# Optimization experiments

Hardware: AMD Instinct MI355X
Metric: run time of the kernel (lower is better)

The kernel has to match this reference:

```python
import jax, jax.numpy as jnp
import numpy as np

B = 65536   # batch
S = 3       # pad_size / seq len
DIN = 72    # input feature dim
D = 100     # dim_model
H = 10      # num_head
DH = D // H # dim_head = 10
FF = 512    # ffn hidden
L = 8       # encoder layers
CLS = 40    # cls_dim


def _pos_encoding():
    pe = np.array([[pos / 10000.0 ** (i // 2 * 2.0 / D) for i in range(D)]
                   for pos in range(S)], dtype=np.float32)
    pe[:, 0::2] = np.sin(pe[:, 0::2])
    pe[:, 1::2] = np.cos(pe[:, 1::2])
    return jnp.asarray(pe)  # [S, D]


def setup_inputs() -> dict:
    key = jax.random.key(0)
    ks = jax.random.split(key, 24)
    n = lambda k, shape: 0.05 * jax.random.normal(k, shape, dtype=jnp.float32)
    inp = {
        'x': jax.random.normal(ks[0], (B, S, DIN), dtype=jnp.float32),
        'label': jax.random.randint(ks[1], (B,), 0, CLS),
        'fa_label': jax.random.randint(ks[2], (B,), 0, CLS),
        'We': n(ks[3], (D, DIN)), 'be': n(ks[4], (D,)),
        'pe': _pos_encoding(),
        'Wq': n(ks[5], (L, D, D)), 'bq': n(ks[6], (L, D)),
        'Wk': n(ks[7], (L, D, D)), 'bk': n(ks[8], (L, D)),
        'Wv': n(ks[9], (L, D, D)), 'bv': n(ks[10], (L, D)),
        'Wo': n(ks[11], (L, D, D)), 'bo': n(ks[12], (L, D)),
        'ln1_g': jnp.ones((L, D), jnp.float32), 'ln1_b': jnp.zeros((L, D), jnp.float32),
        'W1': n(ks[13], (L, FF, D)), 'b1': n(ks[14], (L, FF)),
        'W2': n(ks[15], (L, D, FF)), 'b2': n(ks[16], (L, D)),
        'ln2_g': jnp.ones((L, D), jnp.float32), 'ln2_b': jnp.zeros((L, D), jnp.float32),
        'Wf': n(ks[17], (CLS, S * D)), 'bf': n(ks[18], (CLS,)),
    }
    return inp


def _ln(x, g, b, eps=1e-5):
    m = x.mean(-1, keepdims=True)
    v = ((x - m) ** 2).mean(-1, keepdims=True)
    return (x - m) / jnp.sqrt(v + eps) * g + b


def _forward(x, We, be, pe, Wq, bq, Wk, bk, Wv, bv, Wo, bo,
             ln1_g, ln1_b, W1, b1, W2, b2, ln2_g, ln2_b, Wf, bf):
    Bsz = x.shape[0]
    out = x @ We.T + be          # [B, S, D] embedding
    out = out + pe               # positional encoding (dropout = identity in eval)
    scale = DH ** -0.5
    for i in range(L):
        xin = out
        Q = xin @ Wq[i].T + bq[i]
        K = xin @ Wk[i].T + bk[i]
        V = xin @ Wv[i].T + bv[i]
        # Faithful row-major reshape (original uses .view, which interleaves
        # seq and head dims rather than a transpose-based head split).
        Qh = Q.reshape(Bsz * H, -1, DH)   # [B*H, S, DH]
        Kh = K.reshape(Bsz * H, -1, DH)
        Vh = V.reshape(Bsz * H, -1, DH)
        attn = jax.nn.softmax(jnp.einsum('bqd,bkd->bqk', Qh, Kh) * scale, axis=-1)
        ctx = jnp.einsum('bqk,bkd->bqd', attn, Vh).reshape(Bsz, -1, D)
        out = _ln(ctx @ Wo[i].T + bo[i] + xin, ln1_g[i], ln1_b[i])
        # position-wise FFN
        h = jax.nn.relu(out @ W1[i].T + b1[i])
        out = _ln(h @ W2[i].T + b2[i] + out, ln2_g[i], ln2_b[i])
    out = out.reshape(Bsz, S * D) @ Wf.T + bf   # [B, CLS]
    return out


def reference(x, label, fa_label, We, be, pe, Wq, bq, Wk, bk, Wv, bv, Wo, bo,
              ln1_g, ln1_b, W1, b1, W2, b2, ln2_g, ln2_b, Wf, bf):
    # label / fa_label are unused in the original forward
    return _forward(x, We, be, pe, Wq, bq, Wk, bk, Wv, bv, Wo, bo,
                    ln1_g, ln1_b, W1, b1, W2, b2, ln2_g, ln2_b, Wf, bf)
```

## Files before the change

kernel.cpp:

```cpp
#include <hip/hip_runtime.h>
#include <hip/hip_bf16.h>


typedef __attribute__((ext_vector_type(8))) short short8;
typedef __attribute__((ext_vector_type(4))) float floatx4;

namespace {
constexpr int S = 3, DIN = 72, D = 100, FF = 512, L = 8, CLS = 40;
constexpr int NB = 16, R = 48, NT = 256;
constexpr int LDA = 136;
constexpr int LDH = 200;
constexpr float SCALE = 0.3162277660168379f;

constexpr int PL_QKVO = 7 * 4 * 512;
constexpr int WQ_OFF = 0;
constexpr int WK_OFF = WQ_OFF + L * PL_QKVO;
constexpr int WV_OFF = WK_OFF + L * PL_QKVO;
constexpr int WO_OFF = WV_OFF + L * PL_QKVO;
constexpr int PL_W1 = 32 * 4 * 512;
constexpr int W1_OFF = WO_OFF + L * PL_QKVO;
constexpr int PL_W2 = 7 * 16 * 512;
constexpr int W2_OFF = W1_OFF + L * PL_W1;
constexpr int WE_OFF = W2_OFF + L * PL_W2;
}

__device__ __forceinline__ unsigned short f2bf(float f) {
  unsigned int u = __float_as_uint(f);
  u = u + 0x7fffu + ((u >> 16) & 1u);
  return (unsigned short)(u >> 16);
}

__device__ __forceinline__ unsigned pkbf(float a, float b) {
  __hip_bfloat162 h = __float22bfloat162_rn(make_float2(a, b));
  return *reinterpret_cast<unsigned*>(&h);
}

__device__ __forceinline__ void st_bf4(unsigned short* p, floatx4 v) {
  *reinterpret_cast<uint2*>(p) = make_uint2(pkbf(v.x, v.y), pkbf(v.z, v.w));
}

__device__ __forceinline__ void load10(float* o, const unsigned short* p) {
  const unsigned* u = (const unsigned*)p;
#pragma unroll
  for (int w = 0; w < 5; ++w) {
    unsigned x = u[w];
    o[2 * w] = __uint_as_float(x << 16);
    o[2 * w + 1] = __uint_as_float(x & 0xffff0000u);
  }
}

__device__ __forceinline__ void ldwf4(const unsigned short* base, short8* o) {
#pragma unroll
  for (int ks = 0; ks < 4; ++ks) o[ks] = *(const short8*)(base + ks * 512);
}

__device__ __forceinline__ void ln_rows(float* xrow, const float* srow,
                                        const float* __restrict__ g,
                                        const float* __restrict__ b,
                                        unsigned short* sArow, int ln,
                                        int cnt) {
  floatx4 v[7];
  float sum = 0.f;
#pragma unroll
  for (int i = 0; i < 7; ++i)
    if (i < cnt) {
      const int col = i * 16 + ln * 4;
      floatx4 t = *(const floatx4*)(xrow + col) + *(const floatx4*)(srow + col);
      v[i] = t;
      sum += t.x + t.y + t.z + t.w;
    }
  sum += __shfl_xor(sum, 1, 4);
  sum += __shfl_xor(sum, 2, 4);
  const float mean = sum * 0.01f;
  float var = 0.f;
#pragma unroll
  for (int i = 0; i < 7; ++i)
    if (i < cnt) {
      floatx4 d = v[i] - mean;
      var += d.x * d.x + d.y * d.y + d.z * d.z + d.w * d.w;
    }
  var += __shfl_xor(var, 1, 4);
  var += __shfl_xor(var, 2, 4);
  const float rstd = rsqrtf(var * 0.01f + 1e-5f);
#pragma unroll
  for (int i = 0; i < 7; ++i)
    if (i < cnt) {
      const int col = i * 16 + ln * 4;
      floatx4 o = (v[i] - mean) * rstd * *(const floatx4*)(g + col) +
                  *(const floatx4*)(b + col);
      *(floatx4*)(xrow + col) = o;
      st_bf4(sArow + col, o);
    }
}

__global__ void prep_weights(const float* __restrict__ Wq, const float* __restrict__ Wk,
                             const float* __restrict__ Wv, const float* __restrict__ Wo,
                             const float* __restrict__ W1, const float* __restrict__ W2,
                             const float* __restrict__ We,
                             unsigned short* __restrict__ ws) {
  const int gid = blockIdx.x * 256 + threadIdx.x;
  constexpr int T_QKVO = 8 * 7 * 4 * 64;
  constexpr int T_W1 = 8 * 32 * 4 * 64;
  constexpr int T_W2 = 8 * 7 * 16 * 64;
  constexpr int T_WE = 7 * 3 * 64;
  if (gid >= 4 * T_QKVO + T_W1 + T_W2 + T_WE) return;

  const float* src;
  unsigned short* dst;
  int within, ntc, ksc, N, Ksrc, lstride;
  if (gid < 4 * T_QKVO) {
    const int t = gid / T_QKVO;
    within = gid % T_QKVO;
    src = (t == 0 ? Wq : t == 1 ? Wk : t == 2 ? Wv : Wo);
    dst = ws + (t == 0 ? WQ_OFF : t == 1 ? WK_OFF : t == 2 ? WV_OFF : WO_OFF);
    ntc = 7; ksc = 4; N = 100; Ksrc = 100; lstride = 10000;
  } else if (gid < 4 * T_QKVO + T_W1) {
    within = gid - 4 * T_QKVO;
    src = W1; dst = ws + W1_OFF;
    ntc = 32; ksc = 4; N = 512; Ksrc = 100; lstride = 51200;
  } else if (gid < 4 * T_QKVO + T_W1 + T_W2) {
    within = gid - 4 * T_QKVO - T_W1;
    src = W2; dst = ws + W2_OFF;
    ntc = 7; ksc = 16; N = 100; Ksrc = 512; lstride = 51200;
  } else {
    within = gid - 4 * T_QKVO - T_W1 - T_W2;
    src = We; dst = ws + WE_OFF;
    ntc = 7; ksc = 3; N = 100; Ksrc = 72; lstride = 0;
  }
  const int lane = within & 63;
  int tmp = within >> 6;
  const int ks = tmp % ksc; tmp /= ksc;
  const int nt = tmp % ntc;
  const int lay = tmp / ntc;
  const int n = nt * 16 + (lane & 15);
  const int kb = ks * 32 + (lane >> 4) * 8;
  const float* sp = src + (size_t)lay * lstride + (size_t)n * Ksrc;
  unsigned short o[8];
#pragma unroll
  for (int j = 0; j < 8; ++j) {
    const int k = kb + j;
    float v = (n < N && k < Ksrc) ? sp[k] : 0.f;
    o[j] = f2bf(v);
  }
  uint4 pk = make_uint4((unsigned)o[0] | ((unsigned)o[1] << 16),
                        (unsigned)o[2] | ((unsigned)o[3] << 16),
                        (unsigned)o[4] | ((unsigned)o[5] << 16),
                        (unsigned)o[6] | ((unsigned)o[7] << 16));
  *reinterpret_cast<uint4*>(dst + (size_t)within * 8) = pk;
}

__global__ __launch_bounds__(NT, 3)
void geomap_mfma(const float* __restrict__ gx,
                 const float* __restrict__ be, const float* __restrict__ pe,
                 const float* __restrict__ bq, const float* __restrict__ bk,
                 const float* __restrict__ bv, const float* __restrict__ bo,
                 const float* __restrict__ g1, const float* __restrict__ bt1,
                 const float* __restrict__ b1, const float* __restrict__ b2,
                 const float* __restrict__ g2, const float* __restrict__ bt2,
                 const float* __restrict__ Wf, const float* __restrict__ bfc,
                 const unsigned short* __restrict__ ws,
                 float* __restrict__ gout) {
  __shared__ __align__(16) char smem[51456];
  unsigned short* sA = (unsigned short*)smem;
  float* sXf = (float*)(smem + 13056);
  unsigned short* sQ = (unsigned short*)(smem + 32256);
  unsigned short* sK = (unsigned short*)(smem + 41856);
  float* scr = (float*)(smem + 32256);
  unsigned short* sH = (unsigned short*)(smem + 32256);

  const int tid = threadIdx.x;
  const int lane = tid & 63;
  const int wid = tid >> 6;
  const int l15 = lane & 15;
  const int quad = lane >> 4;
  const int blk = blockIdx.x;

  const int row_o = tid >> 2, ln_o = tid & 3;
  const int cnt_o = (ln_o == 0) ? 7 : 6;

  for (int i = tid; i < R * LDA / 2; i += NT) ((unsigned*)sA)[i] = 0u;
  __syncthreads();
  for (int i = tid; i < R * DIN / 2; i += NT) {
    const int row = i / 36, c = (i % 36) * 2;
    const float2 f2 = *(const float2*)(gx + ((size_t)blk * R + row) * DIN + c);
    ((unsigned*)sA)[row * (LDA / 2) + (c >> 1)] = pkbf(f2.x, f2.y);
  }
  __syncthreads();

  {
    short8 xe[3][3];
#pragma unroll
    for (int mt = 0; mt < 3; ++mt)
#pragma unroll
      for (int ks = 0; ks < 3; ++ks)
        xe[mt][ks] = *(const short8*)(sA + (mt * 16 + l15) * LDA + ks * 32 + quad * 8);
    __syncthreads();
    for (int nt = wid; nt < 7; nt += 4) {
      const unsigned short* wb = ws + WE_OFF + (size_t)(nt * 3) * 512 + (size_t)lane * 8;
      short8 w0 = *(const short8*)(wb);
      short8 w1 = *(const short8*)(wb + 512);
      short8 w2 = *(const short8*)(wb + 1024);
      const int n0 = nt * 16 + quad * 4;
      floatx4 a[3];
#pragma unroll
      for (int mt = 0; mt < 3; ++mt) {
        a[mt] = floatx4{0.f, 0.f, 0.f, 0.f};
        a[mt] = __builtin_amdgcn_mfma_f32_16x16x32_bf16(w0, xe[mt][0], a[mt], 0, 0, 0);
        a[mt] = __builtin_amdgcn_mfma_f32_16x16x32_bf16(w1, xe[mt][1], a[mt], 0, 0, 0);
        a[mt] = __builtin_amdgcn_mfma_f32_16x16x32_bf16(w2, xe[mt][2], a[mt], 0, 0, 0);
      }
      if (n0 < D) {
        const floatx4 bev = *(const floatx4*)(be + n0);
#pragma unroll
        for (int mt = 0; mt < 3; ++mt) {
          const int row = mt * 16 + l15;
          const int s = row % 3;
          const floatx4 pev = *(const floatx4*)(pe + s * D + n0);
          const floatx4 o = a[mt] + bev + pev;
          *(floatx4*)(sXf + row * D + n0) = o;
          st_bf4(sA + row * LDA + n0, o);
        }
      }
    }
  }
  __syncthreads();

  for (int lay = 0; lay < L; ++lay) {
    {
      short8 xf[3][4];
#pragma unroll
      for (int mt = 0; mt < 3; ++mt)
#pragma unroll
        for (int ks = 0; ks < 4; ++ks)
          xf[mt][ks] = *(const short8*)(sA + (mt * 16 + l15) * LDA + ks * 32 + quad * 8);
      __syncthreads();
      const unsigned short* wbase[3] = {ws + WQ_OFF + lay * PL_QKVO,
                                        ws + WK_OFF + lay * PL_QKVO,
                                        ws + WV_OFF + lay * PL_QKVO};
      for (int u = wid; u < 21; u += 4) {
        const int mat = u / 7, nt = u % 7;
        short8 wf[4];
        ldwf4(wbase[mat] + (size_t)nt * 2048 + (size_t)lane * 8, wf);
        const int n0 = nt * 16 + quad * 4;
        floatx4 bias = {0.f, 0.f, 0.f, 0.f};
        const float* bsrc = (mat == 0 ? bq : mat == 1 ? bk : bv) + lay * D;
        if (n0 < D) bias = *(const floatx4*)(bsrc + n0);
        floatx4 a0 = bias, a1 = bias, a2 = bias;
#pragma unroll
        for (int ks = 0; ks < 4; ++ks) {
          a0 = __builtin_amdgcn_mfma_f32_16x16x32_bf16(wf[ks], xf[0][ks], a0, 0, 0, 0);
          a1 = __builtin_amdgcn_mfma_f32_16x16x32_bf16(wf[ks], xf[1][ks], a1, 0, 0, 0);
          a2 = __builtin_amdgcn_mfma_f32_16x16x32_bf16(wf[ks], xf[2][ks], a2, 0, 0, 0);
        }
        if (n0 < D) {
          const floatx4 av[3] = {a0, a1, a2};
#pragma unroll
          for (int mt = 0; mt < 3; ++mt) {
            const int row = mt * 16 + l15;
            if (mat == 0) st_bf4(sQ + row * 100 + n0, av[mt]);
            else if (mat == 1) st_bf4(sK + row * 100 + n0, av[mt]);
            else st_bf4(sA + row * LDA + n0, av[mt]);
          }
        }
      }
    }
    __syncthreads();

    if (tid < 160) {
      const int e = tid / 10, h = tid % 10;
      const unsigned short* Qe = sQ + e * 300;
      const unsigned short* Ke = sK + e * 300;
      float Kv[3][10];
#pragma unroll
      for (int t = 0; t < 3; ++t) load10(Kv[t], Ke + h * 30 + t * 10);
      float p[3][3];
#pragma unroll
      for (int sq = 0; sq < 3; ++sq) {
        float q[10];
        load10(q, Qe + h * 30 + sq * 10);
        float sc[3];
#pragma unroll
        for (int t = 0; t < 3; ++t) {
          float s0 = 0.f;
#pragma unroll
          for (int j = 0; j < 10; ++j) s0 += q[j] * Kv[t][j];
          sc[t] = s0 * SCALE;
        }
        const float m = fmaxf(sc[0], fmaxf(sc[1], sc[2]));
        float p0 = __expf(sc[0] - m), p1 = __expf(sc[1] - m), p2 = __expf(sc[2] - m);
        const float inv = 1.f / (p0 + p1 + p2);
        p[sq][0] = p0 * inv; p[sq][1] = p1 * inv; p[sq][2] = p2 * inv;
      }
      float ctx[3][10];
#pragma unroll
      for (int sq = 0; sq < 3; ++sq)
#pragma unroll
        for (int j = 0; j < 10; ++j) ctx[sq][j] = 0.f;
#pragma unroll
      for (int t = 0; t < 3; ++t) {
        const int pv = h * 30 + t * 10;
        float vv[10];
        load10(vv, sA + (e * 3 + pv / 100) * LDA + (pv % 100));
#pragma unroll
        for (int sq = 0; sq < 3; ++sq)
#pragma unroll
          for (int j = 0; j < 10; ++j) ctx[sq][j] += p[sq][t] * vv[j];
      }
#pragma unroll
      for (int sq = 0; sq < 3; ++sq) {
        const int pq = h * 30 + sq * 10;
        unsigned* dp = (unsigned*)(sA + (e * 3 + pq / 100) * LDA + (pq % 100));
#pragma unroll
        for (int w = 0; w < 5; ++w)
          dp[w] = pkbf(ctx[sq][2 * w], ctx[sq][2 * w + 1]);
      }
    }
    __syncthreads();

    {
      short8 cf[3][4];
#pragma unroll
      for (int mt = 0; mt < 3; ++mt)
#pragma unroll
        for (int ks = 0; ks < 4; ++ks)
          cf[mt][ks] = *(const short8*)(sA + (mt * 16 + l15) * LDA + ks * 32 + quad * 8);
      const unsigned short* wbase = ws + WO_OFF + lay * PL_QKVO;
      for (int u = wid; u < 7; u += 4) {
        short8 wf[4];
        ldwf4(wbase + (size_t)u * 2048 + (size_t)lane * 8, wf);
        const int n0 = u * 16 + quad * 4;
        floatx4 bias = {0.f, 0.f, 0.f, 0.f};
        if (n0 < D) bias = *(const floatx4*)(bo + lay * D + n0);
        floatx4 a0 = bias, a1 = bias, a2 = bias;
#pragma unroll
        for (int ks = 0; ks < 4; ++ks) {
          a0 = __builtin_amdgcn_mfma_f32_16x16x32_bf16(wf[ks], cf[0][ks], a0, 0, 0, 0);
          a1 = __builtin_amdgcn_mfma_f32_16x16x32_bf16(wf[ks], cf[1][ks], a1, 0, 0, 0);
          a2 = __builtin_amdgcn_mfma_f32_16x16x32_bf16(wf[ks], cf[2][ks], a2, 0, 0, 0);
        }
        if (n0 < D) {
          const floatx4 av[3] = {a0, a1, a2};
#pragma unroll
          for (int mt = 0; mt < 3; ++mt)
            *(floatx4*)(scr + (mt * 16 + l15) * D + n0) = av[mt];
        }
      }
    }
    __syncthreads();
    if (tid < 192)
      ln_rows(sXf + row_o * D, scr + row_o * D, g1 + lay * D, bt1 + lay * D,
              sA + row_o * LDA, ln_o, cnt_o);
    __syncthreads();

    {
      short8 ff[3][4];
#pragma unroll
      for (int mt = 0; mt < 3; ++mt)
#pragma unroll
        for (int ks = 0; ks < 4; ++ks)
          ff[mt][ks] = *(const short8*)(sA + (mt * 16 + l15) * LDA + ks * 32 + quad * 8);
      floatx4 facc[2][3];
      const int ntA = wid, ntB = wid + 4;
#pragma unroll
      for (int idx = 0; idx < 2; ++idx) {
        const int nt = idx == 0 ? ntA : ntB;
        const int n0 = nt * 16 + quad * 4;
        floatx4 bias = {0.f, 0.f, 0.f, 0.f};
        if (nt < 7 && n0 < D) bias = *(const floatx4*)(b2 + lay * D + n0);
#pragma unroll
        for (int mt = 0; mt < 3; ++mt) facc[idx][mt] = bias;
      }
      const unsigned short* w1b = ws + W1_OFF + (size_t)lay * PL_W1;
      const unsigned short* w2b = ws + W2_OFF + (size_t)lay * PL_W2;

#pragma unroll
      for (int c = 0; c < 3; ++c) {
        const int base_nt = c * 12;
        const int cnt_nt = (c == 2) ? 8 : 12;
        const int kb = c * 6, ke = kb + ((c == 2) ? 4 : 6);
        for (int l = wid; l < cnt_nt; l += 4) {
          const int ntg = base_nt + l;
          short8 wf[4];
          ldwf4(w1b + (size_t)ntg * 2048 + (size_t)lane * 8, wf);
          const floatx4 b1v = *(const floatx4*)(b1 + lay * FF + ntg * 16 + quad * 4);
          floatx4 a0 = b1v, a1 = b1v, a2 = b1v;
#pragma unroll
          for (int ks = 0; ks < 4; ++ks) {
            a0 = __builtin_amdgcn_mfma_f32_16x16x32_bf16(wf[ks], ff[0][ks], a0, 0, 0, 0);
            a1 = __builtin_amdgcn_mfma_f32_16x16x32_bf16(wf[ks], ff[1][ks], a1, 0, 0, 0);
            a2 = __builtin_amdgcn_mfma_f32_16x16x32_bf16(wf[ks], ff[2][ks], a2, 0, 0, 0);
          }
          const int nloc = l * 16 + quad * 4;
          const floatx4 av[3] = {a0, a1, a2};
#pragma unroll
          for (int mt = 0; mt < 3; ++mt) {
            const int row = mt * 16 + l15;
            floatx4 r;
            r.x = fmaxf(av[mt].x, 0.f); r.y = fmaxf(av[mt].y, 0.f);
            r.z = fmaxf(av[mt].z, 0.f); r.w = fmaxf(av[mt].w, 0.f);
            st_bf4(sH + row * LDH + nloc, r);
          }
        }
        __syncthreads();
        short8 wA = *(const short8*)(w2b + (size_t)(ntA * 16 + kb) * 512 + (size_t)lane * 8);
        short8 wB = wA;
        if (ntB < 7)
          wB = *(const short8*)(w2b + (size_t)(ntB * 16 + kb) * 512 + (size_t)lane * 8);
        for (int ksl = kb; ksl < ke; ++ksl) {
          short8 nA = wA, nB = wB;
          if (ksl + 1 < ke) {
            nA = *(const short8*)(w2b + (size_t)(ntA * 16 + ksl + 1) * 512 + (size_t)lane * 8);
            if (ntB < 7)
              nB = *(const short8*)(w2b + (size_t)(ntB * 16 + ksl + 1) * 512 + (size_t)lane * 8);
          }
          short8 hf[3];
#pragma unroll
          for (int mt = 0; mt < 3; ++mt)
            hf[mt] = *(const short8*)(sH + (mt * 16 + l15) * LDH + (ksl - kb) * 32 + quad * 8);
#pragma unroll
          for (int mt = 0; mt < 3; ++mt)
            facc[0][mt] = __builtin_amdgcn_mfma_f32_16x16x32_bf16(wA, hf[mt], facc[0][mt], 0, 0, 0);
          if (ntB < 7) {
#pragma unroll
            for (int mt = 0; mt < 3; ++mt)
              facc[1][mt] = __builtin_amdgcn_mfma_f32_16x16x32_bf16(wB, hf[mt], facc[1][mt], 0, 0, 0);
          }
          wA = nA; wB = nB;
        }
        __syncthreads();
      }
#pragma unroll
      for (int idx = 0; idx < 2; ++idx) {
        const int nt = idx == 0 ? ntA : ntB;
        const int n0 = nt * 16 + quad * 4;
        if (nt < 7 && n0 < D) {
#pragma unroll
          for (int mt = 0; mt < 3; ++mt)
            *(floatx4*)(scr + (mt * 16 + l15) * D + n0) = facc[idx][mt];
        }
      }
    }
    __syncthreads();
    if (tid < 192)
      ln_rows(sXf + row_o * D, scr + row_o * D, g2 + lay * D, bt2 + lay * D,
              sA + row_o * LDA, ln_o, cnt_o);
    __syncthreads();
  }

  if (tid < 160) {
    const int c = tid % 40, eg = tid / 40;
    float acc[4];
#pragma unroll
    for (int i = 0; i < 4; ++i) acc[i] = bfc[c];
    const floatx4* wr = (const floatx4*)(Wf + c * 300);
    for (int kq = 0; kq < 75; ++kq) {
      const floatx4 w4 = wr[kq];
#pragma unroll
      for (int i = 0; i < 4; ++i) {
        const floatx4 x4 = *(const floatx4*)(sXf + (eg * 4 + i) * 300 + kq * 4);
        acc[i] += w4.x * x4.x + w4.y * x4.y + w4.z * x4.z + w4.w * x4.w;
      }
    }
#pragma unroll
    for (int i = 0; i < 4; ++i)
      gout[((size_t)blk * NB + eg * 4 + i) * CLS + c] = acc[i];
  }
}

extern "C" void kernel_launch(void* const* d_in, const int* in_sizes, int n_in,
                              void* d_out, int out_size, void* d_ws,
                              size_t ws_size, hipStream_t stream) {
  const float* x   = (const float*)d_in[0];
  const float* We  = (const float*)d_in[3];
  const float* be  = (const float*)d_in[4];
  const float* pe  = (const float*)d_in[5];
  const float* Wq  = (const float*)d_in[6];
  const float* bq  = (const float*)d_in[7];
  const float* Wk  = (const float*)d_in[8];
  const float* bk  = (const float*)d_in[9];
  const float* Wv  = (const float*)d_in[10];
  const float* bv  = (const float*)d_in[11];
  const float* Wo  = (const float*)d_in[12];
  const float* bo  = (const float*)d_in[13];
  const float* g1  = (const float*)d_in[14];
  const float* bt1 = (const float*)d_in[15];
  const float* W1  = (const float*)d_in[16];
  const float* b1  = (const float*)d_in[17];
  const float* W2  = (const float*)d_in[18];
  const float* b2  = (const float*)d_in[19];
  const float* g2  = (const float*)d_in[20];
  const float* bt2 = (const float*)d_in[21];
  const float* Wf  = (const float*)d_in[22];
  const float* bf  = (const float*)d_in[23];
  float* out = (float*)d_out;
  unsigned short* ws = (unsigned short*)d_ws;

  prep_weights<<<710, 256, 0, stream>>>(Wq, Wk, Wv, Wo, W1, W2, We, ws);

  const int B = in_sizes[0] / (S * DIN);
  const int blocks = B / NB;
  geomap_mfma<<<blocks, 256, 0, stream>>>(x, be, pe, bq, bk, bv, bo,
                                          g1, bt1, b1, b2, g2, bt2, Wf, bf,
                                          ws, out);
}
```

Before: 1.367 ms.

## Double block size to 512 threads and split attention per query row

Raises the fused transformer kernel's block from 4 to 8 wavefronts and redistributes every MFMA tile loop across 8 waves. In the FFN, each wave now owns a single W2 output tile instead of two. Attention work moves from 160 threads handling all 3 query rows each to 480 threads handling one row each, with an extra barrier before writing context back into shared memory. This aims for more parallelism per block and lower per-thread latency, but many phases still have only 7 tiles, so extra waves sit idle. Occupancy is now bounded by registers at 6 waves-per-EU launch bounds.

After: 3.416 ms. 2.5x slower.

```diff
diff --git a/kernel.cpp b/kernel.cpp
--- a/kernel.cpp
+++ b/kernel.cpp
@@ -7,7 +7,7 @@
 
 namespace {
 constexpr int S = 3, DIN = 72, D = 100, FF = 512, L = 8, CLS = 40;
-constexpr int NB = 16, R = 48, NT = 256;
+constexpr int NB = 16, R = 48, NT = 512;
 constexpr int LDA = 136;
 constexpr int LDH = 200;
 constexpr float SCALE = 0.3162277660168379f;
@@ -149,7 +149,7 @@
   *reinterpret_cast<uint4*>(dst + (size_t)within * 8) = pk;
 }
 
-__global__ __launch_bounds__(NT, 3)
+__global__ __launch_bounds__(NT, 6)
 void geomap_mfma(const float* __restrict__ gx,
                  const float* __restrict__ be, const float* __restrict__ pe,
                  const float* __restrict__ bq, const float* __restrict__ bk,
@@ -195,7 +195,7 @@
       for (int ks = 0; ks < 3; ++ks)
         xe[mt][ks] = *(const short8*)(sA + (mt * 16 + l15) * LDA + ks * 32 + quad * 8);
     __syncthreads();
-    for (int nt = wid; nt < 7; nt += 4) {
+    for (int nt = wid; nt < 7; nt += 8) {
       const unsigned short* wb = ws + WE_OFF + (size_t)(nt * 3) * 512 + (size_t)lane * 8;
       short8 w0 = *(const short8*)(wb);
       short8 w1 = *(const short8*)(wb + 512);
@@ -237,7 +237,7 @@
       const unsigned short* wbase[3] = {ws + WQ_OFF + lay * PL_QKVO,
                                         ws + WK_OFF + lay * PL_QKVO,
                                         ws + WV_OFF + lay * PL_QKVO};
-      for (int u = wid; u < 21; u += 4) {
+      for (int u = wid; u < 21; u += 8) {
         const int mat = u / 7, nt = u % 7;
         short8 wf[4];
         ldwf4(wbase[mat] + (size_t)nt * 2048 + (size_t)lane * 8, wf);
@@ -266,54 +266,48 @@
     }
     __syncthreads();
 
-    if (tid < 160) {
-      const int e = tid / 10, h = tid % 10;
+    float actx[10];
+    int a_e = 0, a_pq = 0;
+    const bool a_on = tid < 480;
+    if (a_on) {
+      const int e = tid / 30, hq = tid % 30;
+      const int h = hq / 3, sq = hq % 3;
       const unsigned short* Qe = sQ + e * 300;
       const unsigned short* Ke = sK + e * 300;
-      float Kv[3][10];
-#pragma unroll
-      for (int t = 0; t < 3; ++t) load10(Kv[t], Ke + h * 30 + t * 10);
-      float p[3][3];
-#pragma unroll
-      for (int sq = 0; sq < 3; ++sq) {
-        float q[10];
-        load10(q, Qe + h * 30 + sq * 10);
-        float sc[3];
-#pragma unroll
-        for (int t = 0; t < 3; ++t) {
-          float s0 = 0.f;
-#pragma unroll
-          for (int j = 0; j < 10; ++j) s0 += q[j] * Kv[t][j];
-          sc[t] = s0 * SCALE;
-        }
-        const float m = fmaxf(sc[0], fmaxf(sc[1], sc[2]));
-        float p0 = __expf(sc[0] - m), p1 = __expf(sc[1] - m), p2 = __expf(sc[2] - m);
-        const float inv = 1.f / (p0 + p1 + p2);
-        p[sq][0] = p0 * inv; p[sq][1] = p1 * inv; p[sq][2] = p2 * inv;
-      }
-      float ctx[3][10];
-#pragma unroll
-      for (int sq = 0; sq < 3; ++sq)
-#pragma unroll
-        for (int j = 0; j < 10; ++j) ctx[sq][j] = 0.f;
+      float q[10];
+      load10(q, Qe + h * 30 + sq * 10);
+      float sc[3];
+#pragma unroll
+      for (int t = 0; t < 3; ++t) {
+        float kv[10];
+        load10(kv, Ke + h * 30 + t * 10);
+        float s0 = 0.f;
+#pragma unroll
+        for (int j = 0; j < 10; ++j) s0 += q[j] * kv[j];
+        sc[t] = s0 * SCALE;
+      }
+      const float m = fmaxf(sc[0], fmaxf(sc[1], sc[2]));
+      float p0 = __expf(sc[0] - m), p1 = __expf(sc[1] - m), p2 = __expf(sc[2] - m);
+      const float inv = 1.f / (p0 + p1 + p2);
+      const float p[3] = {p0 * inv, p1 * inv, p2 * inv};
+#pragma unroll
+      for (int j = 0; j < 10; ++j) actx[j] = 0.f;
 #pragma unroll
       for (int t = 0; t < 3; ++t) {
         const int pv = h * 30 + t * 10;
         float vv[10];
         load10(vv, sA + (e * 3 + pv / 100) * LDA + (pv % 100));
 #pragma unroll
-        for (int sq = 0; sq < 3; ++sq)
-#pragma unroll
-          for (int j = 0; j < 10; ++j) ctx[sq][j] += p[sq][t] * vv[j];
-      }
-#pragma unroll
-      for (int sq = 0; sq < 3; ++sq) {
-        const int pq = h * 30 + sq * 10;
-        unsigned* dp = (unsigned*)(sA + (e * 3 + pq / 100) * LDA + (pq % 100));
-#pragma unroll
-        for (int w = 0; w < 5; ++w)
-          dp[w] = pkbf(ctx[sq][2 * w], ctx[sq][2 * w + 1]);
-      }
+        for (int j = 0; j < 10; ++j) actx[j] += p[t] * vv[j];
+      }
+      a_e = e; a_pq = h * 30 + sq * 10;
+    }
+    __syncthreads();
+    if (a_on) {
+      unsigned* dp = (unsigned*)(sA + (a_e * 3 + a_pq / 100) * LDA + (a_pq % 100));
+#pragma unroll
+      for (int w = 0; w < 5; ++w)
+        dp[w] = pkbf(actx[2 * w], actx[2 * w + 1]);
     }
     __syncthreads();
 
@@ -325,7 +319,7 @@
         for (int ks = 0; ks < 4; ++ks)
           cf[mt][ks] = *(const short8*)(sA + (mt * 16 + l15) * LDA + ks * 32 + quad * 8);
       const unsigned short* wbase = ws + WO_OFF + lay * PL_QKVO;
-      for (int u = wid; u < 7; u += 4) {
+      for (int u = wid; u < 7; u += 8) {
         short8 wf[4];
         ldwf4(wbase + (size_t)u * 2048 + (size_t)lane * 8, wf);
         const int n0 = u * 16 + quad * 4;
@@ -359,16 +353,15 @@
 #pragma unroll
         for (int ks = 0; ks < 4; ++ks)
           ff[mt][ks] = *(const short8*)(sA + (mt * 16 + l15) * LDA + ks * 32 + quad * 8);
-      floatx4 facc[2][3];
-      const int ntA = wid, ntB = wid + 4;
-#pragma unroll
-      for (int idx = 0; idx < 2; ++idx) {
-        const int nt = idx == 0 ? ntA : ntB;
-        const int n0 = nt * 16 + quad * 4;
+      floatx4 facc[3];
+      const int ntA = wid;
+      const bool actA = ntA < 7;
+      {
+        const int n0 = ntA * 16 + quad * 4;
         floatx4 bias = {0.f, 0.f, 0.f, 0.f};
-        if (nt < 7 && n0 < D) bias = *(const floatx4*)(b2 + lay * D + n0);
-#pragma unroll
-        for (int mt = 0; mt < 3; ++mt) facc[idx][mt] = bias;
+        if (actA && n0 < D) bias = *(const floatx4*)(b2 + lay * D + n0);
+#pragma unroll
+        for (int mt = 0; mt < 3; ++mt) facc[mt] = bias;
       }
       const unsigned short* w1b = ws + W1_OFF + (size_t)lay * PL_W1;
       const unsigned short* w2b = ws + W2_OFF + (size_t)lay * PL_W2;
@@ -378,7 +371,7 @@
         const int base_nt = c * 12;
         const int cnt_nt = (c == 2) ? 8 : 12;
         const int kb = c * 6, ke = kb + ((c == 2) ? 4 : 6);
-        for (int l = wid; l < cnt_nt; l += 4) {
+        for (int l = wid; l < cnt_nt; l += 8) {
           const int ntg = base_nt + l;
           short8 wf[4];
           ldwf4(w1b + (size_t)ntg * 2048 + (size_t)lane * 8, wf);
@@ -402,41 +395,30 @@
           }
         }
         __syncthreads();
-        short8 wA = *(const short8*)(w2b + (size_t)(ntA * 16 + kb) * 512 + (size_t)lane * 8);
-        short8 wB = wA;
-        if (ntB < 7)
-          wB = *(const short8*)(w2b + (size_t)(ntB * 16 + kb) * 512 + (size_t)lane * 8);
-        for (int ksl = kb; ksl < ke; ++ksl) {
-          short8 nA = wA, nB = wB;
-          if (ksl + 1 < ke) {
-            nA = *(const short8*)(w2b + (size_t)(ntA * 16 + ksl + 1) * 512 + (size_t)lane * 8);
-            if (ntB < 7)
-              nB = *(const short8*)(w2b + (size_t)(ntB * 16 + ksl + 1) * 512 + (size_t)lane * 8);
+        if (actA) {
+          short8 wA = *(const short8*)(w2b + (size_t)(ntA * 16 + kb) * 512 + (size_t)lane * 8);
+          for (int ksl = kb; ksl < ke; ++ksl) {
+            short8 nA = wA;
+            if (ksl + 1 < ke)
+              nA = *(const short8*)(w2b + (size_t)(ntA * 16 + ksl + 1) * 512 + (size_t)lane * 8);
+            short8 hf[3];
+#pragma unroll
+            for (int mt = 0; mt < 3; ++mt)
+              hf[mt] = *(const short8*)(sH + (mt * 16 + l15) * LDH + (ksl - kb) * 32 + quad * 8);
+#pragma unroll
+            for (int mt = 0; mt < 3; ++mt)
+              facc[mt] = __builtin_amdgcn_mfma_f32_16x16x32_bf16(wA, hf[mt], facc[mt], 0, 0, 0);
+            wA = nA;
           }
-          short8 hf[3];
+        }
+        __syncthreads();
+      }
+      if (actA) {
+        const int n0 = ntA * 16 + quad * 4;
+        if (n0 < D) {
 #pragma unroll
           for (int mt = 0; mt < 3; ++mt)
-            hf[mt] = *(const short8*)(sH + (mt * 16 + l15) * LDH + (ksl - kb) * 32 + quad * 8);
-#pragma unroll
-          for (int mt = 0; mt < 3; ++mt)
-            facc[0][mt] = __builtin_amdgcn_mfma_f32_16x16x32_bf16(wA, hf[mt], facc[0][mt], 0, 0, 0);
-          if (ntB < 7) {
-#pragma unroll
-            for (int mt = 0; mt < 3; ++mt)
-              facc[1][mt] = __builtin_amdgcn_mfma_f32_16x16x32_bf16(wB, hf[mt], facc[1][mt], 0, 0, 0);
-          }
-          wA = nA; wB = nB;
-        }
-        __syncthreads();
-      }
-#pragma unroll
-      for (int idx = 0; idx < 2; ++idx) {
-        const int nt = idx == 0 ? ntA : ntB;
-        const int n0 = nt * 16 + quad * 4;
-        if (nt < 7 && n0 < D) {
-#pragma unroll
-          for (int mt = 0; mt < 3; ++mt)
-            *(floatx4*)(scr + (mt * 16 + l15) * D + n0) = facc[idx][mt];
+            *(floatx4*)(scr + (mt * 16 + l15) * D + n0) = facc[mt];
         }
       }
     }
@@ -499,7 +481,7 @@
 
   const int B = in_sizes[0] / (S * DIN);
   const int blocks = B / NB;
-  geomap_mfma<<<blocks, 256, 0, stream>>>(x, be, pe, bq, bk, bv, bo,
-                                          g1, bt1, b1, b2, g2, bt2, Wf, bf,
-                                          ws, out);
-}
+  geomap_mfma<<<blocks, NT, 0, stream>>>(x, be, pe, bq, bk, bv, bo,
+                                         g1, bt1, b1, b2, g2, bt2, Wf, bf,
+                                         ws, out);
+}
```

## Software-pipeline weight fragment loads across GEMM stages and raise MFMA priority

Applied to the files above, without the earlier changes.

Weight fragments for the QKV, Wo, FFN1 and next-layer Q GEMMs are now prefetched into registers one step ahead. The prefetches are issued before barriers, attention and layernorm, so global/L2 latency overlaps with other work instead of stalling each unit. MFMA sequences are wrapped in s_setprio to favour matrix issue among the co-resident waves. The cost is more live vector registers, which may lower occupancy or cause spills.

Measured after the change: 1.656 ms. 21.2% more time.

```diff
diff --git a/kernel.cpp b/kernel.cpp
--- a/kernel.cpp
+++ b/kernel.cpp
@@ -49,10 +49,115 @@
   }
 }
 
-__device__ __forceinline__ void ldwf4(const unsigned short* base, short8* o) {
-#pragma unroll
-  for (int ks = 0; ks < 4; ++ks) o[ks] = *(const short8*)(base + ks * 512);
-}
+#define LDW4(P, V0, V1, V2, V3)               \
+  do {                                        \
+    const unsigned short* _wpp = (P);         \
+    V0 = *(const short8*)(_wpp);              \
+    V1 = *(const short8*)(_wpp + 512);        \
+    V2 = *(const short8*)(_wpp + 1024);       \
+    V3 = *(const short8*)(_wpp + 1536);       \
+  } while (0)
+
+#define MFMA_BF16 __builtin_amdgcn_mfma_f32_16x16x32_bf16
+
+#define QKV_UNIT(U, A0, A1, A2, A3)                                \
+  do {                                                             \
+    const int _u = (U);                                            \
+    const int _mat = _u / 7, _nt = _u % 7;                         \
+    const int _n0 = _nt * 16 + quad * 4;                           \
+    const float* _bs = (_mat == 0 ? bq : _mat == 1 ? bk : bv) + lay * D; \
+    floatx4 _b = {0.f, 0.f, 0.f, 0.f};                             \
+    if (_n0 < D) _b = *(const floatx4*)(_bs + _n0);                \
+    floatx4 _a0 = _b, _a1 = _b, _a2 = _b;                          \
+    __builtin_amdgcn_s_setprio(1);                                 \
+    _a0 = MFMA_BF16(A0, xf[0][0], _a0, 0, 0, 0);                   \
+    _a1 = MFMA_BF16(A0, xf[1][0], _a1, 0, 0, 0);                   \
+    _a2 = MFMA_BF16(A0, xf[2][0], _a2, 0, 0, 0);                   \
+    _a0 = MFMA_BF16(A1, xf[0][1], _a0, 0, 0, 0);                   \
+    _a1 = MFMA_BF16(A1, xf[1][1], _a1, 0, 0, 0);                   \
+    _a2 = MFMA_BF16(A1, xf[2][1], _a2, 0, 0, 0);                   \
+    _a0 = MFMA_BF16(A2, xf[0][2], _a0, 0, 0, 0);                   \
+    _a1 = MFMA_BF16(A2, xf[1][2], _a1, 0, 0, 0);                   \
+    _a2 = MFMA_BF16(A2, xf[2][2], _a2, 0, 0, 0);                   \
+    _a0 = MFMA_BF16(A3, xf[0][3], _a0, 0, 0, 0);                   \
+    _a1 = MFMA_BF16(A3, xf[1][3], _a1, 0, 0, 0);                   \
+    _a2 = MFMA_BF16(A3, xf[2][3], _a2, 0, 0, 0);                   \
+    __builtin_amdgcn_s_setprio(0);                                 \
+    if (_n0 < D) {                                                 \
+      if (_mat == 0) {                                             \
+        st_bf4(sQ + (l15) * 100 + _n0, _a0);                       \
+        st_bf4(sQ + (16 + l15) * 100 + _n0, _a1);                  \
+        st_bf4(sQ + (32 + l15) * 100 + _n0, _a2);                  \
+      } else if (_mat == 1) {                                      \
+        st_bf4(sK + (l15) * 100 + _n0, _a0);                       \
+        st_bf4(sK + (16 + l15) * 100 + _n0, _a1);                  \
+        st_bf4(sK + (32 + l15) * 100 + _n0, _a2);                  \
+      } else {                                                     \
+        st_bf4(sA + (l15)*LDA + _n0, _a0);                         \
+        st_bf4(sA + (16 + l15) * LDA + _n0, _a1);                  \
+        st_bf4(sA + (32 + l15) * LDA + _n0, _a2);                  \
+      }                                                            \
+    }                                                              \
+  } while (0)
+
+#define WO_UNIT(U, A0, A1, A2, A3)                                 \
+  do {                                                             \
+    const int _n0 = (U) * 16 + quad * 4;                           \
+    floatx4 _b = {0.f, 0.f, 0.f, 0.f};                             \
+    if (_n0 < D) _b = *(const floatx4*)(bo + lay * D + _n0);       \
+    floatx4 _a0 = _b, _a1 = _b, _a2 = _b;                          \
+    __builtin_amdgcn_s_setprio(1);                                 \
+    _a0 = MFMA_BF16(A0, cf[0][0], _a0, 0, 0, 0);                   \
+    _a1 = MFMA_BF16(A0, cf[1][0], _a1, 0, 0, 0);                   \
+    _a2 = MFMA_BF16(A0, cf[2][0], _a2, 0, 0, 0);                   \
+    _a0 = MFMA_BF16(A1, cf[0][1], _a0, 0, 0, 0);                   \
+    _a1 = MFMA_BF16(A1, cf[1][1], _a1, 0, 0, 0);                   \
+    _a2 = MFMA_BF16(A1, cf[2][1], _a2, 0, 0, 0);                   \
+    _a0 = MFMA_BF16(A2, cf[0][2], _a0, 0, 0, 0);                   \
+    _a1 = MFMA_BF16(A2, cf[1][2], _a1, 0, 0, 0);                   \
+    _a2 = MFMA_BF16(A2, cf[2][2], _a2, 0, 0, 0);                   \
+    _a0 = MFMA_BF16(A3, cf[0][3], _a0, 0, 0, 0);                   \
+    _a1 = MFMA_BF16(A3, cf[1][3], _a1, 0, 0, 0);                   \
+    _a2 = MFMA_BF16(A3, cf[2][3], _a2, 0, 0, 0);                   \
+    __builtin_amdgcn_s_setprio(0);                                 \
+    if (_n0 < D) {                                                 \
+      *(floatx4*)(scr + (l15)*D + _n0) = _a0;                      \
+      *(floatx4*)(scr + (16 + l15) * D + _n0) = _a1;               \
+      *(floatx4*)(scr + (32 + l15) * D + _n0) = _a2;               \
+    }                                                              \
+  } while (0)
+
+#define FFN1_UNIT(LL, A0, A1, A2, A3)                              \
+  do {                                                             \
+    const int _l = (LL), _ntg = base_nt + _l;                      \
+    const floatx4 _bv = *(const floatx4*)(b1 + lay * FF + _ntg * 16 + quad * 4); \
+    floatx4 _a0 = _bv, _a1 = _bv, _a2 = _bv;                       \
+    __builtin_amdgcn_s_setprio(1);                                 \
+    _a0 = MFMA_BF16(A0, ff[0][0], _a0, 0, 0, 0);                   \
+    _a1 = MFMA_BF16(A0, ff[1][0], _a1, 0, 0, 0);                   \
+    _a2 = MFMA_BF16(A0, ff[2][0], _a2, 0, 0, 0);                   \
+    _a0 = MFMA_BF16(A1, ff[0][1], _a0, 0, 0, 0);                   \
+    _a1 = MFMA_BF16(A1, ff[1][1], _a1, 0, 0, 0);                   \
+    _a2 = MFMA_BF16(A1, ff[2][1], _a2, 0, 0, 0);                   \
+    _a0 = MFMA_BF16(A2, ff[0][2], _a0, 0, 0, 0);                   \
+    _a1 = MFMA_BF16(A2, ff[1][2], _a1, 0, 0, 0);                   \
+    _a2 = MFMA_BF16(A2, ff[2][2], _a2, 0, 0, 0);                   \
+    _a0 = MFMA_BF16(A3, ff[0][3], _a0, 0, 0, 0);                   \
+    _a1 = MFMA_BF16(A3, ff[1][3], _a1, 0, 0, 0);                   \
+    _a2 = MFMA_BF16(A3, ff[2][3], _a2, 0, 0, 0);                   \
+    __builtin_amdgcn_s_setprio(0);                                 \
+    const int _nl = _l * 16 + quad * 4;                            \
+    floatx4 _r;                                                    \
+    _r.x = fmaxf(_a0.x, 0.f); _r.y = fmaxf(_a0.y, 0.f);            \
+    _r.z = fmaxf(_a0.z, 0.f); _r.w = fmaxf(_a0.w, 0.f);            \
+    st_bf4(sH + (l15)*LDH + _nl, _r);                              \
+    _r.x = fmaxf(_a1.x, 0.f); _r.y = fmaxf(_a1.y, 0.f);            \
+    _r.z = fmaxf(_a1.z, 0.f); _r.w = fmaxf(_a1.w, 0.f);            \
+    st_bf4(sH + (16 + l15) * LDH + _nl, _r);                       \
+    _r.x = fmaxf(_a2.x, 0.f); _r.y = fmaxf(_a2.y, 0.f);            \
+    _r.z = fmaxf(_a2.z, 0.f); _r.w = fmaxf(_a2.w, 0.f);            \
+    st_bf4(sH + (32 + l15) * LDH + _nl, _r);                       \
+  } while (0)
 
 __device__ __forceinline__ void ln_rows(float* xrow, const float* srow,
                                         const float* __restrict__ g,
@@ -178,6 +283,8 @@
   const int row_o = tid >> 2, ln_o = tid & 3;
   const int cnt_o = (ln_o == 0) ? 7 : 6;
 
+  short8 qw0, qw1, qw2, qw3;
+
   for (int i = tid; i < R * LDA / 2; i += NT) ((unsigned*)sA)[i] = 0u;
   __syncthreads();
   for (int i = tid; i < R * DIN / 2; i += NT) {
@@ -202,13 +309,15 @@
       short8 w2 = *(const short8*)(wb + 1024);
       const int n0 = nt * 16 + quad * 4;
       floatx4 a[3];
+      __builtin_amdgcn_s_setprio(1);
 #pragma unroll
       for (int mt = 0; mt < 3; ++mt) {
         a[mt] = floatx4{0.f, 0.f, 0.f, 0.f};
-        a[mt] = __builtin_amdgcn_mfma_f32_16x16x32_bf16(w0, xe[mt][0], a[mt], 0, 0, 0);
-        a[mt] = __builtin_amdgcn_mfma_f32_16x16x32_bf16(w1, xe[mt][1], a[mt], 0, 0, 0);
-        a[mt] = __builtin_amdgcn_mfma_f32_16x16x32_bf16(w2, xe[mt][2], a[mt], 0, 0, 0);
-      }
+        a[mt] = MFMA_BF16(w0, xe[mt][0], a[mt], 0, 0, 0);
+        a[mt] = MFMA_BF16(w1, xe[mt][1], a[mt], 0, 0, 0);
+        a[mt] = MFMA_BF16(w2, xe[mt][2], a[mt], 0, 0, 0);
+      }
+      __builtin_amdgcn_s_setprio(0);
       if (n0 < D) {
         const floatx4 bev = *(const floatx4*)(be + n0);
 #pragma unroll
@@ -223,10 +332,22 @@
       }
     }
   }
+  LDW4(ws + WQ_OFF + (size_t)wid * 2048 + (size_t)lane * 8, qw0, qw1, qw2, qw3);
   __syncthreads();
 
   for (int lay = 0; lay < L; ++lay) {
+    const unsigned short* w1b = ws + W1_OFF + (size_t)lay * PL_W1;
+    const unsigned short* w2b = ws + W2_OFF + (size_t)lay * PL_W2;
+
     {
+      const unsigned short* wqb = ws + WQ_OFF + lay * PL_QKVO;
+      const unsigned short* wkb = ws + WK_OFF + lay * PL_QKVO;
+      const unsigned short* wvb = ws + WV_OFF + lay * PL_QKVO;
+      auto wp = [&](int u) {
+        const int mat = u / 7, nt = u % 7;
+        const unsigned short* bse = (mat == 0) ? wqb : (mat == 1) ? wkb : wvb;
+        return bse + (size_t)nt * 2048 + (size_t)lane * 8;
+      };
       short8 xf[3][4];
 #pragma unroll
       for (int mt = 0; mt < 3; ++mt)
@@ -234,37 +355,25 @@
         for (int ks = 0; ks < 4; ++ks)
           xf[mt][ks] = *(const short8*)(sA + (mt * 16 + l15) * LDA + ks * 32 + quad * 8);
       __syncthreads();
-      const unsigned short* wbase[3] = {ws + WQ_OFF + lay * PL_QKVO,
-                                        ws + WK_OFF + lay * PL_QKVO,
-                                        ws + WV_OFF + lay * PL_QKVO};
-      for (int u = wid; u < 21; u += 4) {
-        const int mat = u / 7, nt = u % 7;
-        short8 wf[4];
-        ldwf4(wbase[mat] + (size_t)nt * 2048 + (size_t)lane * 8, wf);
-        const int n0 = nt * 16 + quad * 4;
-        floatx4 bias = {0.f, 0.f, 0.f, 0.f};
-        const float* bsrc = (mat == 0 ? bq : mat == 1 ? bk : bv) + lay * D;
-        if (n0 < D) bias = *(const floatx4*)(bsrc + n0);
-        floatx4 a0 = bias, a1 = bias, a2 = bias;
-#pragma unroll
-        for (int ks = 0; ks < 4; ++ks) {
-          a0 = __builtin_amdgcn_mfma_f32_16x16x32_bf16(wf[ks], xf[0][ks], a0, 0, 0, 0);
-          a1 = __builtin_amdgcn_mfma_f32_16x16x32_bf16(wf[ks], xf[1][ks], a1, 0, 0, 0);
-          a2 = __builtin_amdgcn_mfma_f32_16x16x32_bf16(wf[ks], xf[2][ks], a2, 0, 0, 0);
-        }
-        if (n0 < D) {
-          const floatx4 av[3] = {a0, a1, a2};
-#pragma unroll
-          for (int mt = 0; mt < 3; ++mt) {
-            const int row = mt * 16 + l15;
-            if (mat == 0) st_bf4(sQ + row * 100 + n0, av[mt]);
-            else if (mat == 1) st_bf4(sK + row * 100 + n0, av[mt]);
-            else st_bf4(sA + row * LDA + n0, av[mt]);
-          }
-        }
-      }
-    }
-    __syncthreads();
+      short8 t0, t1, t2, t3, r0, r1, r2, r3;
+      LDW4(wp(wid + 4), t0, t1, t2, t3);
+      LDW4(wp(wid + 8), r0, r1, r2, r3);
+      QKV_UNIT(wid, qw0, qw1, qw2, qw3);
+      LDW4(wp(wid + 12), qw0, qw1, qw2, qw3);
+      QKV_UNIT(wid + 4, t0, t1, t2, t3);
+      LDW4(wp(wid + 16), t0, t1, t2, t3);
+      QKV_UNIT(wid + 8, r0, r1, r2, r3);
+      const bool last = (wid + 20) < 21;
+      if (last) LDW4(wp(wid + 20), r0, r1, r2, r3);
+      QKV_UNIT(wid + 12, qw0, qw1, qw2, qw3);
+      QKV_UNIT(wid + 16, t0, t1, t2, t3);
+      if (last) QKV_UNIT(wid + 20, r0, r1, r2, r3);
+    }
+    __syncthreads();
+
+    short8 p0, p1, p2, p3;
+    LDW4(ws + WO_OFF + (size_t)lay * PL_QKVO + (size_t)wid * 2048 +
+             (size_t)lane * 8, p0, p1, p2, p3);
 
     if (tid < 160) {
       const int e = tid / 10, h = tid % 10;
@@ -287,9 +396,9 @@
           sc[t] = s0 * SCALE;
         }
         const float m = fmaxf(sc[0], fmaxf(sc[1], sc[2]));
-        float p0 = __expf(sc[0] - m), p1 = __expf(sc[1] - m), p2 = __expf(sc[2] - m);
-        const float inv = 1.f / (p0 + p1 + p2);
-        p[sq][0] = p0 * inv; p[sq][1] = p1 * inv; p[sq][2] = p2 * inv;
+        float p0e = __expf(sc[0] - m), p1e = __expf(sc[1] - m), p2e = __expf(sc[2] - m);
+        const float inv = 1.f / (p0e + p1e + p2e);
+        p[sq][0] = p0e * inv; p[sq][1] = p1e * inv; p[sq][2] = p2e * inv;
       }
       float ctx[3][10];
 #pragma unroll
@@ -324,29 +433,19 @@
 #pragma unroll
         for (int ks = 0; ks < 4; ++ks)
           cf[mt][ks] = *(const short8*)(sA + (mt * 16 + l15) * LDA + ks * 32 + quad * 8);
-      const unsigned short* wbase = ws + WO_OFF + lay * PL_QKVO;
-      for (int u = wid; u < 7; u += 4) {
-        short8 wf[4];
-        ldwf4(wbase + (size_t)u * 2048 + (size_t)lane * 8, wf);
-        const int n0 = u * 16 + quad * 4;
-        floatx4 bias = {0.f, 0.f, 0.f, 0.f};
-        if (n0 < D) bias = *(const floatx4*)(bo + lay * D + n0);
-        floatx4 a0 = bias, a1 = bias, a2 = bias;
-#pragma unroll
-        for (int ks = 0; ks < 4; ++ks) {
-          a0 = __builtin_amdgcn_mfma_f32_16x16x32_bf16(wf[ks], cf[0][ks], a0, 0, 0, 0);
-          a1 = __builtin_amdgcn_mfma_f32_16x16x32_bf16(wf[ks], cf[1][ks], a1, 0, 0, 0);
-          a2 = __builtin_amdgcn_mfma_f32_16x16x32_bf16(wf[ks], cf[2][ks], a2, 0, 0, 0);
-        }
-        if (n0 < D) {
-          const floatx4 av[3] = {a0, a1, a2};
-#pragma unroll
-          for (int mt = 0; mt < 3; ++mt)
-            *(floatx4*)(scr + (mt * 16 + l15) * D + n0) = av[mt];
-        }
-      }
-    }
-    __syncthreads();
+      const unsigned short* wob = ws + WO_OFF + lay * PL_QKVO;
+      const bool u2on = (wid + 4) < 7;
+      short8 s0, s1, s2, s3;
+      if (u2on)
+        LDW4(wob + (size_t)(wid + 4) * 2048 + (size_t)lane * 8, s0, s1, s2, s3);
+      WO_UNIT(wid, p0, p1, p2, p3);
+      if (u2on) WO_UNIT(wid + 4, s0, s1, s2, s3);
+    }
+    __syncthreads();
+
+    short8 f0, f1, f2, f3;
+    LDW4(w1b + (size_t)wid * 2048 + (size_t)lane * 8, f0, f1, f2, f3);
+
     if (tid < 192)
       ln_rows(sXf + row_o * D, scr + row_o * D, g1 + lay * D, bt1 + lay * D,
               sA + row_o * LDA, ln_o, cnt_o);
@@ -370,42 +469,28 @@
 #pragma unroll
         for (int mt = 0; mt < 3; ++mt) facc[idx][mt] = bias;
       }
-      const unsigned short* w1b = ws + W1_OFF + (size_t)lay * PL_W1;
-      const unsigned short* w2b = ws + W2_OFF + (size_t)lay * PL_W2;
 
 #pragma unroll
       for (int c = 0; c < 3; ++c) {
         const int base_nt = c * 12;
-        const int cnt_nt = (c == 2) ? 8 : 12;
         const int kb = c * 6, ke = kb + ((c == 2) ? 4 : 6);
-        for (int l = wid; l < cnt_nt; l += 4) {
-          const int ntg = base_nt + l;
-          short8 wf[4];
-          ldwf4(w1b + (size_t)ntg * 2048 + (size_t)lane * 8, wf);
-          const floatx4 b1v = *(const floatx4*)(b1 + lay * FF + ntg * 16 + quad * 4);
-          floatx4 a0 = b1v, a1 = b1v, a2 = b1v;
-#pragma unroll
-          for (int ks = 0; ks < 4; ++ks) {
-            a0 = __builtin_amdgcn_mfma_f32_16x16x32_bf16(wf[ks], ff[0][ks], a0, 0, 0, 0);
-            a1 = __builtin_amdgcn_mfma_f32_16x16x32_bf16(wf[ks], ff[1][ks], a1, 0, 0, 0);
-            a2 = __builtin_amdgcn_mfma_f32_16x16x32_bf16(wf[ks], ff[2][ks], a2, 0, 0, 0);
-          }
-          const int nloc = l * 16 + quad * 4;
-          const floatx4 av[3] = {a0, a1, a2};
-#pragma unroll
-          for (int mt = 0; mt < 3; ++mt) {
-            const int row = mt * 16 + l15;
-            floatx4 r;
-            r.x = fmaxf(av[mt].x, 0.f); r.y = fmaxf(av[mt].y, 0.f);
-            r.z = fmaxf(av[mt].z, 0.f); r.w = fmaxf(av[mt].w, 0.f);
-            st_bf4(sH + row * LDH + nloc, r);
-          }
-        }
-        __syncthreads();
+        short8 y0, y1, y2, y3;
+        LDW4(w1b + (size_t)(base_nt + wid + 4) * 2048 + (size_t)lane * 8,
+             y0, y1, y2, y3);
+        FFN1_UNIT(wid, f0, f1, f2, f3);
+        if (c < 2)
+          LDW4(w1b + (size_t)(base_nt + wid + 8) * 2048 + (size_t)lane * 8,
+               f0, f1, f2, f3);
+        FFN1_UNIT(wid + 4, y0, y1, y2, y3);
+        if (c < 2) FFN1_UNIT(wid + 8, f0, f1, f2, f3);
         short8 wA = *(const short8*)(w2b + (size_t)(ntA * 16 + kb) * 512 + (size_t)lane * 8);
         short8 wB = wA;
         if (ntB < 7)
           wB = *(const short8*)(w2b + (size_t)(ntB * 16 + kb) * 512 + (size_t)lane * 8);
+        __syncthreads();
+        if (c < 2)
+          LDW4(w1b + (size_t)(base_nt + 12 + wid) * 2048 + (size_t)lane * 8,
+               f0, f1, f2, f3);
         for (int ksl = kb; ksl < ke; ++ksl) {
           short8 nA = wA, nB = wB;
           if (ksl + 1 < ke) {
@@ -413,18 +498,20 @@
             if (ntB < 7)
               nB = *(const short8*)(w2b + (size_t)(ntB * 16 + ksl + 1) * 512 + (size_t)lane * 8);
           }
-          short8 hf[3];
-#pragma unroll
-          for (int mt = 0; mt < 3; ++mt)
-            hf[mt] = *(const short8*)(sH + (mt * 16 + l15) * LDH + (ksl - kb) * 32 + quad * 8);
-#pragma unroll
-          for (int mt = 0; mt < 3; ++mt)
-            facc[0][mt] = __builtin_amdgcn_mfma_f32_16x16x32_bf16(wA, hf[mt], facc[0][mt], 0, 0, 0);
+          const int koff = (ksl - kb) * 32 + quad * 8;
+          short8 hf0 = *(const short8*)(sH + (l15)*LDH + koff);
+          short8 hf1 = *(const short8*)(sH + (16 + l15) * LDH + koff);
+          short8 hf2 = *(const short8*)(sH + (32 + l15) * LDH + koff);
+          __builtin_amdgcn_s_setprio(1);
+          facc[0][0] = MFMA_BF16(wA, hf0, facc[0][0], 0, 0, 0);
+          facc[0][1] = MFMA_BF16(wA, hf1, facc[0][1], 0, 0, 0);
+          facc[0][2] = MFMA_BF16(wA, hf2, facc[0][2], 0, 0, 0);
           if (ntB < 7) {
-#pragma unroll
-            for (int mt = 0; mt < 3; ++mt)
-              facc[1][mt] = __builtin_amdgcn_mfma_f32_16x16x32_bf16(wB, hf[mt], facc[1][mt], 0, 0, 0);
+            facc[1][0] = MFMA_BF16(wB, hf0, facc[1][0], 0, 0, 0);
+            facc[1][1] = MFMA_BF16(wB, hf1, facc[1][1], 0, 0, 0);
+            facc[1][2] = MFMA_BF16(wB, hf2, facc[1][2], 0, 0, 0);
           }
+          __builtin_amdgcn_s_setprio(0);
           wA = nA; wB = nB;
         }
         __syncthreads();
@@ -441,6 +528,11 @@
       }
     }
     __syncthreads();
+
+    if (lay + 1 < L)
+      LDW4(ws + WQ_OFF + (size_t)(lay + 1) * PL_QKVO + (size_t)wid * 2048 +
+               (size_t)lane * 8, qw0, qw1, qw2, qw3);
+
     if (tid < 192)
       ln_rows(sXf + row_o * D, scr + row_o * D, g2 + lay * D, bt2 + lay * D,
               sA + row_o * LDA, ln_o, cnt_o);
@@ -499,7 +591,7 @@
 
   const int B = in_sizes[0] / (S * DIN);
   const int blocks = B / NB;
-  geomap_mfma<<<blocks, 256, 0, stream>>>(x, be, pe, bq, bk, bv, bo,
-                                          g1, bt1, b1, b2, g2, bt2, Wf, bf,
-                                          ws, out);
-}
+  geomap_mfma<<<blocks, NT, 0, stream>>>(x, be, pe, bq, bk, bv, bo,
+                                         g1, bt1, b1, b2, g2, bt2, Wf, bf,
+                                         ws, out);
+}
```
